# Kernel optimization log

Hardware: AMD Instinct MI355X
Metric: run time of the kernel (lower is better)

## Reference

```python
import jax, jax.numpy as jnp
import numpy as np


def setup_inputs() -> dict:
    key = jax.random.key(0)
    k1, k2 = jax.random.split(key)
    B, T, D, K = 8, 4096, 256, 1024
    z = jax.random.normal(k1, (B, T, D), dtype=jnp.float32)
    codebook = jax.random.uniform(k2, (K, D), dtype=jnp.float32)
    return {"z": z, "codebook": codebook}


def reference(z, codebook):
    # Squared L2 distance via dot-product decomposition (same argmin as
    # the broadcasted squared-difference in the original module, without
    # materializing the (B,T,K,D) intermediate).
    #   ||z - c||^2 = ||z||^2 - 2 z.c + ||c||^2
    z_sq = jnp.sum(z * z, axis=-1, keepdims=True)            # (B,T,1)
    c_sq = jnp.sum(codebook * codebook, axis=-1)             # (K,)
    cross = jnp.einsum("btd,kd->btk", z, codebook)           # (B,T,K)
    l2_distance = z_sq - 2.0 * cross + c_sq                  # (B,T,K)
    codebook_indices = jnp.argmin(l2_distance, axis=-1)      # (B,T)
    z_q = codebook[codebook_indices]                         # (B,T,D)
    # Straight-through estimator
    z_q = z + jax.lax.stop_gradient(z_q - z)
    return (z_q, codebook_indices)
```

## Files before the change

kernel.cpp:

```cpp
#include <hip/hip_runtime.h>
#include <math.h>

#define NTOK   32768
#define NDIM   256
#define NCODE  1024
#define CHUNK  4096

typedef _Float16 f16x8 __attribute__((ext_vector_type(8)));
typedef float    f32x4 __attribute__((ext_vector_type(4)));

__device__ __forceinline__ void gld_lds16(const void* g, void* l) {
    __builtin_amdgcn_global_load_lds(
        (const __attribute__((address_space(1))) void*)g,
        (__attribute__((address_space(3))) void*)l, 16, 0, 0);
}

__global__ __launch_bounds__(256) void prep_cb(
        const float* __restrict__ cb,
        _Float16* __restrict__ ch, _Float16* __restrict__ cl,
        float* __restrict__ csq) {
    const int L   = blockIdx.x * 256 + threadIdx.x;
    const int row = L >> 5;
    const int g   = L & 31;

    const float* src = cb + (size_t)row * NDIM + g * 8;
    float4 a0 = *(const float4*)src;
    float4 a1 = *(const float4*)(src + 4);
    float v[8] = {a0.x, a0.y, a0.z, a0.w, a1.x, a1.y, a1.z, a1.w};
    f16x8 hi, lo;
    float s = 0.f;
    #pragma unroll
    for (int e = 0; e < 8; ++e) {
        _Float16 h = (_Float16)v[e];
        hi[e] = h;
        lo[e] = (_Float16)(v[e] - (float)h);
        s += v[e] * v[e];
    }
    const int r = row & 127;
    const size_t dst = (size_t)((row >> 7) * 8 + (g >> 2)) * CHUNK
                     + (r >> 4) * 512 + (g & 3) * 128 + (r & 15) * 8;
    *(f16x8*)&ch[dst] = hi;
    *(f16x8*)&cl[dst] = lo;
    #pragma unroll
    for (int off = 16; off > 0; off >>= 1) s += __shfl_down(s, off, 32);
    if ((threadIdx.x & 31) == 0) csq[row] = s;
}


#define PHASE(p, GB, DOSTAGE, WK, FIRSTZ) do {                               \
    const int _sl = (p) & 3;                                                 \
    f16x8 fbh[4], fbl[4];                                                    \
    _Pragma("unroll")                                                        \
    for (int _t = 0; _t < 4; ++_t) {                                         \
        fbh[_t] = *(const f16x8*)&Bs[_sl][0][boff[_t]];                      \
        fbl[_t] = *(const f16x8*)&Bs[_sl][1][boff[_t]];                      \
    }                                                                        \
    if (DOSTAGE) {                                                           \
        const size_t _s  = (size_t)((GB) + (p) + 3) * CHUNK + tid * 8;       \
        const int    _dsl = ((p) + 3) & 3;                                   \
        const int    _d   = tid * 8;                                         \
        gld_lds16(ch + _s,        &Bs[_dsl][0][_d]);                         \
        gld_lds16(ch + _s + 2048, &Bs[_dsl][0][_d + 2048]);                  \
        gld_lds16(cl + _s,        &Bs[_dsl][1][_d]);                         \
        gld_lds16(cl + _s + 2048, &Bs[_dsl][1][_d + 2048]);                  \
    }                                                                        \
    asm volatile("s_waitcnt vmcnt(" #WK ")" ::: "memory");                   \
    __builtin_amdgcn_s_barrier();                                            \
    asm volatile("s_waitcnt lgkmcnt(0)" ::: "memory");                       \
    __builtin_amdgcn_s_setprio(1);                                           \
    _Pragma("unroll")                                                        \
    for (int _mt = 0; _mt < 2; ++_mt)                                        \
        _Pragma("unroll")                                                    \
        for (int _t = 0; _t < 4; ++_t) {                                     \
            acc[_mt][_t] = __builtin_amdgcn_mfma_f32_16x16x32_f16(           \
                ah[_mt][(p)], fbh[_t],                                       \
                (FIRSTZ) ? zz : acc[_mt][_t], 0, 0, 0);                      \
            acc[_mt][_t] = __builtin_amdgcn_mfma_f32_16x16x32_f16(           \
                al[_mt][(p)], fbh[_t], acc[_mt][_t], 0, 0, 0);               \
            acc[_mt][_t] = __builtin_amdgcn_mfma_f32_16x16x32_f16(           \
                ah[_mt][(p)], fbl[_t], acc[_mt][_t], 0, 0, 0);               \
        }                                                                    \
    __builtin_amdgcn_s_setprio(0);                                           \
    __builtin_amdgcn_s_barrier();                                            \
} while (0)

#define FOLD(S) do {                                                         \
    float cs[4];                                                             \
    _Pragma("unroll")                                                        \
    for (int _t = 0; _t < 4; ++_t)                                           \
        cs[_t] = csq_lds[(S) * 128 + (nx * 4 + _t) * 16 + lr];               \
    _Pragma("unroll")                                                        \
    for (int _mt = 0; _mt < 2; ++_mt)                                        \
        _Pragma("unroll")                                                    \
        for (int _r = 0; _r < 4; ++_r)                                       \
            _Pragma("unroll")                                                \
            for (int _t = 0; _t < 4; ++_t) {                                 \
                float _v = cs[_t] - 2.0f * acc[_mt][_t][_r];                 \
                int   _n = (S) * 128 + (nx * 4 + _t) * 16 + lr;              \
                if (_v < bv[_mt][_r] ||                                      \
                    (_v == bv[_mt][_r] && _n < bi[_mt][_r])) {               \
                    bv[_mt][_r] = _v; bi[_mt][_r] = _n;                      \
                }                                                            \
            }                                                                \
} while (0)

__global__ __launch_bounds__(256, 2) void vq_main(
        const float* __restrict__ z,
        const _Float16* __restrict__ ch, const _Float16* __restrict__ cl,
        const float* __restrict__ csq, const float* __restrict__ cb,
        float* __restrict__ zq, float* __restrict__ io) {
    __shared__ _Float16 Bs[4][2][4096];
    __shared__ float    csq_lds[1024];

    const int tid  = threadIdx.x;
    const int w    = tid >> 6;
    const int lane = tid & 63;
    const int quad = lane >> 4, lr = lane & 15;
    const int my   = w >> 1, nx = w & 1;
    const int m0   = blockIdx.x * 64;

    gld_lds16(csq + tid * 4, &csq_lds[tid * 4]);
    #pragma unroll
    for (int c = 0; c < 3; ++c) {
        const size_t sb = (size_t)c * CHUNK + tid * 8;
        gld_lds16(ch + sb,        &Bs[c][0][tid * 8]);
        gld_lds16(ch + sb + 2048, &Bs[c][0][tid * 8 + 2048]);
        gld_lds16(cl + sb,        &Bs[c][1][tid * 8]);
        gld_lds16(cl + sb + 2048, &Bs[c][1][tid * 8 + 2048]);
    }

    f16x8 ah[2][8], al[2][8];
    #pragma unroll
    for (int mt = 0; mt < 2; ++mt) {
        const float* zp = z + (size_t)(m0 + my * 32 + mt * 16 + lr) * NDIM
                        + quad * 8;
        #pragma unroll
        for (int c = 0; c < 8; ++c) {
            float4 a0 = *(const float4*)(zp + c * 32);
            float4 a1 = *(const float4*)(zp + c * 32 + 4);
            float v[8] = {a0.x, a0.y, a0.z, a0.w, a1.x, a1.y, a1.z, a1.w};
            #pragma unroll
            for (int e = 0; e < 8; ++e) {
                _Float16 h = (_Float16)v[e];
                ah[mt][c][e] = h;
                al[mt][c][e] = (_Float16)(v[e] - (float)h);
            }
        }
    }

    int boff[4];
    #pragma unroll
    for (int t = 0; t < 4; ++t)
        boff[t] = (nx * 4 + t) * 512 + quad * 128 + lr * 8;

    float bv[2][4];
    int   bi[2][4];
    #pragma unroll
    for (int mt = 0; mt < 2; ++mt)
        #pragma unroll
        for (int r = 0; r < 4; ++r) { bv[mt][r] = INFINITY; bi[mt][r] = 0x7fffffff; }

    const f32x4 zz = (f32x4){0.f, 0.f, 0.f, 0.f};
    f32x4 acc[2][4];
    #pragma unroll
    for (int mt = 0; mt < 2; ++mt)
        #pragma unroll
        for (int t = 0; t < 4; ++t) acc[mt][t] = zz;

    asm volatile("s_waitcnt vmcnt(0)" ::: "memory");
    __syncthreads();

    for (int s = 0; s < 7; ++s) {
        const int gb = s * 8;
        PHASE(0, gb, 1, 8, 1);
        PHASE(1, gb, 1, 8, 0);
        PHASE(2, gb, 1, 8, 0);
        PHASE(3, gb, 1, 8, 0);
        PHASE(4, gb, 1, 8, 0);
        PHASE(5, gb, 1, 8, 0);
        PHASE(6, gb, 1, 8, 0);
        PHASE(7, gb, 1, 8, 0);
        FOLD(s);
    }
    {
        const int gb = 56;
        PHASE(0, gb, 1, 8, 1);
        PHASE(1, gb, 1, 8, 0);
        PHASE(2, gb, 1, 8, 0);
        PHASE(3, gb, 1, 8, 0);
        PHASE(4, gb, 1, 8, 0);
        PHASE(5, gb, 0, 4, 0);
        PHASE(6, gb, 0, 0, 0);
        PHASE(7, gb, 0, 0, 0);
        FOLD(7);
    }

    #pragma unroll
    for (int msk = 1; msk < 16; msk <<= 1)
        #pragma unroll
        for (int mt = 0; mt < 2; ++mt)
            #pragma unroll
            for (int r = 0; r < 4; ++r) {
                float ov = __shfl_xor(bv[mt][r], msk, 64);
                int   oi = __shfl_xor(bi[mt][r], msk, 64);
                if (ov < bv[mt][r] || (ov == bv[mt][r] && oi < bi[mt][r])) {
                    bv[mt][r] = ov; bi[mt][r] = oi;
                }
            }

    __syncthreads();
    float* sval  = (float*)&Bs[0][0][0];
    int*   sidx  = (int*)&Bs[0][0][512];
    int*   bestS = (int*)&Bs[0][0][1024];

    if (lr == 0) {
        #pragma unroll
        for (int mt = 0; mt < 2; ++mt)
            #pragma unroll
            for (int r = 0; r < 4; ++r) {
                int row = my * 32 + mt * 16 + quad * 4 + r;
                sval[row * 2 + nx] = bv[mt][r];
                sidx[row * 2 + nx] = bi[mt][r];
            }
    }
    __syncthreads();

    if (tid < 64) {
        float v0 = sval[tid * 2], v1 = sval[tid * 2 + 1];
        int   i0 = sidx[tid * 2], i1 = sidx[tid * 2 + 1];
        bool take1 = (v1 < v0) || (v1 == v0 && i1 < i0);
        int best = take1 ? i1 : i0;
        bestS[tid] = best;
        io[m0 + tid] = (float)best;
    }
    __syncthreads();

    const int tr = tid >> 4, tc = tid & 15;
    #pragma unroll
    for (int p = 0; p < 4; ++p) {
        int row = p * 16 + tr;
        const float* src = cb + (size_t)bestS[row] * NDIM;
        float*       dst = zq + (size_t)(m0 + row) * NDIM;
        #pragma unroll
        for (int q = 0; q < 4; ++q) {
            int col = q * 64 + tc * 4;
            *(float4*)&dst[col] = *(const float4*)&src[col];
        }
    }
}

extern "C" void kernel_launch(void* const* d_in, const int* in_sizes, int n_in,
                              void* d_out, int out_size, void* d_ws, size_t ws_size,
                              hipStream_t stream) {
    const float* z  = (const float*)d_in[0];
    const float* cb = (const float*)d_in[1];

    float* zq = (float*)d_out;
    float* io = (float*)d_out + (size_t)NTOK * NDIM;

    _Float16* ch  = (_Float16*)d_ws;
    _Float16* cl  = ch + (size_t)NCODE * NDIM;
    float*    csq = (float*)(cl + (size_t)NCODE * NDIM);

    prep_cb<<<NCODE * 32 / 256, 256, 0, stream>>>(cb, ch, cl, csq);

    vq_main<<<NTOK / 64, 256, 0, stream>>>(z, ch, cl, csq, cb, zq, io);
}
```

Before: 133.9 us.

## Prefetch next codebook chunk fragments into registers during MFMA phase

Restructures the main loop so each phase reads the next chunk's B fragments from LDS into a second register set while the MFMAs consume the current set. LDS waits move to the end of each phase. Staging now runs four chunks ahead, with per-wave contiguous 512-element copies, and codebook staging is issued after the z conversion. The aim is to hide LDS read latency behind MFMA work, at the cost of more registers under a 2-blocks-per-CU launch bound.

```diff
diff --git a/kernel.cpp b/kernel.cpp
--- a/kernel.cpp
+++ b/kernel.cpp
@@ -47,40 +47,41 @@
 }
 
 
-#define PHASE(p, GB, DOSTAGE, WK, FIRSTZ) do {                               \
-    const int _sl = (p) & 3;                                                 \
-    f16x8 fbh[4], fbl[4];                                                    \
-    _Pragma("unroll")                                                        \
-    for (int _t = 0; _t < 4; ++_t) {                                         \
-        fbh[_t] = *(const f16x8*)&Bs[_sl][0][boff[_t]];                      \
-        fbl[_t] = *(const f16x8*)&Bs[_sl][1][boff[_t]];                      \
-    }                                                                        \
-    if (DOSTAGE) {                                                           \
-        const size_t _s  = (size_t)((GB) + (p) + 3) * CHUNK + tid * 8;       \
-        const int    _dsl = ((p) + 3) & 3;                                   \
-        const int    _d   = tid * 8;                                         \
-        gld_lds16(ch + _s,        &Bs[_dsl][0][_d]);                         \
-        gld_lds16(ch + _s + 2048, &Bs[_dsl][0][_d + 2048]);                  \
-        gld_lds16(cl + _s,        &Bs[_dsl][1][_d]);                         \
-        gld_lds16(cl + _s + 2048, &Bs[_dsl][1][_d + 2048]);                  \
-    }                                                                        \
+#define STAGE(c, sl) do {                                                    \
+    const size_t _s = (size_t)(c) * CHUNK + w * 1024 + lane * 8;             \
+    const int    _d = w * 1024 + lane * 8;                                   \
+    gld_lds16(ch + _s,       &Bs[sl][0][_d]);                                \
+    gld_lds16(ch + _s + 512, &Bs[sl][0][_d + 512]);                          \
+    gld_lds16(cl + _s,       &Bs[sl][1][_d]);                                \
+    gld_lds16(cl + _s + 512, &Bs[sl][1][_d + 512]);                          \
+} while (0)
+
+#define PHASE(ph, S, FAH, FAL, FBH, FBL, DOSTAGE, WK, FIRSTZ, DOREAD) do {   \
+    if (DOSTAGE) STAGE((S) * 8 + (ph) + 4, (ph) & 3);                        \
     asm volatile("s_waitcnt vmcnt(" #WK ")" ::: "memory");                   \
     __builtin_amdgcn_s_barrier();                                            \
-    asm volatile("s_waitcnt lgkmcnt(0)" ::: "memory");                       \
+    if (DOREAD) {                                                            \
+        _Pragma("unroll")                                                    \
+        for (int _t = 0; _t < 4; ++_t) {                                     \
+            FBH[_t] = *(const f16x8*)&Bs[((ph) + 1) & 3][0][boff[_t]];       \
+            FBL[_t] = *(const f16x8*)&Bs[((ph) + 1) & 3][1][boff[_t]];       \
+        }                                                                    \
+    }                                                                        \
     __builtin_amdgcn_s_setprio(1);                                           \
     _Pragma("unroll")                                                        \
     for (int _mt = 0; _mt < 2; ++_mt)                                        \
         _Pragma("unroll")                                                    \
         for (int _t = 0; _t < 4; ++_t) {                                     \
             acc[_mt][_t] = __builtin_amdgcn_mfma_f32_16x16x32_f16(           \
-                ah[_mt][(p)], fbh[_t],                                       \
+                ah[_mt][(ph)], FAH[_t],                                      \
                 (FIRSTZ) ? zz : acc[_mt][_t], 0, 0, 0);                      \
             acc[_mt][_t] = __builtin_amdgcn_mfma_f32_16x16x32_f16(           \
-                al[_mt][(p)], fbh[_t], acc[_mt][_t], 0, 0, 0);               \
+                al[_mt][(ph)], FAH[_t], acc[_mt][_t], 0, 0, 0);              \
             acc[_mt][_t] = __builtin_amdgcn_mfma_f32_16x16x32_f16(           \
-                ah[_mt][(p)], fbl[_t], acc[_mt][_t], 0, 0, 0);               \
+                ah[_mt][(ph)], FAL[_t], acc[_mt][_t], 0, 0, 0);              \
         }                                                                    \
     __builtin_amdgcn_s_setprio(0);                                           \
+    asm volatile("s_waitcnt lgkmcnt(0)" ::: "memory");                       \
     __builtin_amdgcn_s_barrier();                                            \
 } while (0)
 
@@ -119,16 +120,6 @@
     const int my   = w >> 1, nx = w & 1;
     const int m0   = blockIdx.x * 64;
 
-    gld_lds16(csq + tid * 4, &csq_lds[tid * 4]);
-    #pragma unroll
-    for (int c = 0; c < 3; ++c) {
-        const size_t sb = (size_t)c * CHUNK + tid * 8;
-        gld_lds16(ch + sb,        &Bs[c][0][tid * 8]);
-        gld_lds16(ch + sb + 2048, &Bs[c][0][tid * 8 + 2048]);
-        gld_lds16(cl + sb,        &Bs[c][1][tid * 8]);
-        gld_lds16(cl + sb + 2048, &Bs[c][1][tid * 8 + 2048]);
-    }
-
     f16x8 ah[2][8], al[2][8];
     #pragma unroll
     for (int mt = 0; mt < 2; ++mt) {
@@ -148,6 +139,12 @@
         }
     }
 
+    gld_lds16(csq + tid * 4, &csq_lds[tid * 4]);
+    STAGE(0, 0);
+    STAGE(1, 1);
+    STAGE(2, 2);
+    STAGE(3, 3);
+
     int boff[4];
     #pragma unroll
     for (int t = 0; t < 4; ++t)
@@ -170,28 +167,34 @@
     asm volatile("s_waitcnt vmcnt(0)" ::: "memory");
     __syncthreads();
 
+    f16x8 f0h[4], f0l[4], f1h[4], f1l[4];
+    #pragma unroll
+    for (int t = 0; t < 4; ++t) {
+        f0h[t] = *(const f16x8*)&Bs[0][0][boff[t]];
+        f0l[t] = *(const f16x8*)&Bs[0][1][boff[t]];
+    }
+
     for (int s = 0; s < 7; ++s) {
-        const int gb = s * 8;
-        PHASE(0, gb, 1, 8, 1);
-        PHASE(1, gb, 1, 8, 0);
-        PHASE(2, gb, 1, 8, 0);
-        PHASE(3, gb, 1, 8, 0);
-        PHASE(4, gb, 1, 8, 0);
-        PHASE(5, gb, 1, 8, 0);
-        PHASE(6, gb, 1, 8, 0);
-        PHASE(7, gb, 1, 8, 0);
+        PHASE(0, s, f0h, f0l, f1h, f1l, 1, 12, 1, 1);
+        PHASE(1, s, f1h, f1l, f0h, f0l, 1, 12, 0, 1);
+        PHASE(2, s, f0h, f0l, f1h, f1l, 1, 12, 0, 1);
+        PHASE(3, s, f1h, f1l, f0h, f0l, 1, 12, 0, 1);
+        PHASE(4, s, f0h, f0l, f1h, f1l, 1, 12, 0, 1);
+        PHASE(5, s, f1h, f1l, f0h, f0l, 1, 12, 0, 1);
+        PHASE(6, s, f0h, f0l, f1h, f1l, 1, 12, 0, 1);
+        PHASE(7, s, f1h, f1l, f0h, f0l, 1, 12, 0, 1);
         FOLD(s);
     }
     {
-        const int gb = 56;
-        PHASE(0, gb, 1, 8, 1);
-        PHASE(1, gb, 1, 8, 0);
-        PHASE(2, gb, 1, 8, 0);
-        PHASE(3, gb, 1, 8, 0);
-        PHASE(4, gb, 1, 8, 0);
-        PHASE(5, gb, 0, 4, 0);
-        PHASE(6, gb, 0, 0, 0);
-        PHASE(7, gb, 0, 0, 0);
+        const int s = 7;
+        PHASE(0, s, f0h, f0l, f1h, f1l, 1, 12, 1, 1);
+        PHASE(1, s, f1h, f1l, f0h, f0l, 1, 12, 0, 1);
+        PHASE(2, s, f0h, f0l, f1h, f1l, 1, 12, 0, 1);
+        PHASE(3, s, f1h, f1l, f0h, f0l, 1, 12, 0, 1);
+        PHASE(4, s, f0h, f0l, f1h, f1l, 0,  8, 0, 1);
+        PHASE(5, s, f1h, f1l, f0h, f0l, 0,  4, 0, 1);
+        PHASE(6, s, f0h, f0l, f1h, f1l, 0,  0, 0, 1);
+        PHASE(7, s, f1h, f1l, f0h, f0l, 0,  0, 0, 0);
         FOLD(7);
     }
 
```

Result: slower. 166.7 us (+24.5%).
